# Optimization experiments

Hardware: AMD Instinct MI355X
Metric: run time of the kernel (lower is better)

Reference implementation:

```python
import jax, jax.numpy as jnp
import numpy as np

N_INST = 524288   # total instances across all bags
NF = 256          # feature dim
L = 128           # gated-attention hidden dim
C = 1             # num_classes
B = 4096          # num bags


def setup_inputs() -> dict:
    key = jax.random.key(0)
    k = jax.random.split(key, 6)
    # ragged bag sizes averaging ~128, deterministically summing to N_INST
    rng = np.random.RandomState(0)
    raw = rng.randint(64, 193, size=B).astype(np.int64)
    sizes = (raw * N_INST // raw.sum()).astype(np.int64)
    sizes[: int(N_INST - sizes.sum())] += 1  # distribute remainder (< B)
    assert sizes.sum() == N_INST
    s = 1.0 / np.sqrt(NF)
    return {
        "feats": jax.random.normal(k[0], (N_INST, NF), jnp.float32),
        "split_sizes": jnp.asarray(sizes, jnp.int64),
        "W_ins": jax.random.normal(k[1], (NF, C), jnp.float32) * s,
        "b_ins": jnp.zeros((C,), jnp.float32),
        "W_V": jax.random.normal(k[2], (NF, L), jnp.float32) * s,
        "b_V": jnp.zeros((L,), jnp.float32),
        "W_U": jax.random.normal(k[3], (NF, L), jnp.float32) * s,
        "b_U": jnp.zeros((L,), jnp.float32),
        "w_att": jax.random.normal(k[4], (L, 1), jnp.float32) * (1.0 / np.sqrt(L)),
        "b_att": jnp.zeros((1,), jnp.float32),
    }


def reference(feats, split_sizes, W_ins, b_ins, W_V, b_V, W_U, b_U, w_att, b_att):
    n = feats.shape[0]
    num_bags = split_sizes.shape[0]
    # segment id per instance (fused replacement of torch.split + Python loop)
    seg = jnp.repeat(jnp.arange(num_bags), split_sizes, total_repeat_length=n)

    # instance classifier (applied once to the whole ragged batch)
    inst_pred = feats @ W_ins + b_ins                      # [N, C]

    # gated attention scores
    gate = jnp.tanh(feats @ W_V + b_V) * jax.nn.sigmoid(feats @ W_U + b_U)
    scores = (gate @ w_att + b_att)[:, 0]                  # [N]

    # segmented softmax over each bag
    m = jax.ops.segment_max(scores, seg, num_segments=num_bags)  # [B]
    e = jnp.exp(scores - m[seg])
    denom = jax.ops.segment_sum(e, seg, num_segments=num_bags)   # [B]
    attn = e / denom[seg]                                        # [N]

    # bag prediction = attention-weighted sum of instance predictions
    bag_pred = jax.ops.segment_sum(attn[:, None] * inst_pred, seg,
                                   num_segments=num_bags)        # [B, C]
    return bag_pred, inst_pred
```

## Files before the change

kernel.cpp:

```cpp
#include <hip/hip_runtime.h>
#include <hip/hip_bf16.h>

#define N_INST 524288
#define NF     256
#define LDIM   128
#define NBAGS  4096

typedef __attribute__((ext_vector_type(8)))  short          short8;
typedef __attribute__((ext_vector_type(16))) float          f32x16;
typedef __attribute__((ext_vector_type(4)))  unsigned short ushort4v;
typedef __attribute__((ext_vector_type(4)))  int            int4v;

__device__ __forceinline__ unsigned short f2bf(float f) {
    unsigned u = __float_as_uint(f);
    unsigned r = u + 0x7FFFu + ((u >> 16) & 1u);
    return (unsigned short)(r >> 16);
}

__global__ __launch_bounds__(256) void k_build(const float* __restrict__ W_V,
                                               const float* __restrict__ W_U,
                                               unsigned short* __restrict__ Bws) {
    int idx  = blockIdx.x * 256 + threadIdx.x;
    int j    = idx & 7;
    int lane = (idx >> 3) & 63;
    int ct   = (idx >> 9) & 7;
    int ks   = idx >> 12;
    int k    = ks * 16 + ((lane >> 5) << 3) + j;
    int n    = ((ct >> 1) << 5) + (lane & 31);
    const float* src = (ct & 1) ? W_U : W_V;
    Bws[idx] = f2bf(src[k * LDIM + n]);
}

__global__ __launch_bounds__(256) void k_scan(const int* __restrict__ sraw,
                                              int* __restrict__ offs) {
    __shared__ int csum[256];
    __shared__ int cpref[256];
    const int t = threadIdx.x;
    const bool is64 = (sraw[1] == 0);
    int local[16];
    int ssum = 0;
    for (int j = 0; j < 16; ++j) {
        int i = t * 16 + j;
        int v = is64 ? sraw[2 * i] : sraw[i];
        local[j] = v;
        ssum += v;
    }
    csum[t] = ssum;
    __syncthreads();
    if (t == 0) {
        int run = 0;
        for (int i = 0; i < 256; ++i) { cpref[i] = run; run += csum[i]; }
    }
    __syncthreads();
    int run = cpref[t];
    for (int j = 0; j < 16; ++j) { offs[t * 16 + j] = run; run += local[j]; }
    if (t == 255) offs[NBAGS] = run;
}

__global__ __launch_bounds__(256, 3) void k_gemm(
    const float* __restrict__ feats, const unsigned short* __restrict__ Bws,
    const float* __restrict__ W_ins, const float* __restrict__ b_ins,
    const float* __restrict__ b_V,   const float* __restrict__ b_U,
    const float* __restrict__ w_att, const float* __restrict__ b_att,
    float* __restrict__ scores, float* __restrict__ inst_out) {

    __shared__ unsigned short Al[1024];
    __shared__ unsigned short Bl[4096];
    __shared__ float winsl[NF];
    __shared__ float bVl[LDIM], bUl[LDIM], wal[LDIM];
    __shared__ float Sp[64][4];

    const int t    = threadIdx.x;
    const int lane = t & 63;
    const int cg   = t >> 6;
    const int row  = t >> 2;
    const int seg  = t & 3;
    const long r0  = (long)blockIdx.x * 64;

    winsl[t] = W_ins[t];
    if (t < LDIM) { bVl[t] = b_V[t]; bUl[t] = b_U[t]; wal[t] = w_att[t]; }

    f32x16 acc[2][2] = {};
    float pacc = 0.f;

    const float* arow = feats + (r0 + row) * NF + seg * 4;
    const int4v* bsrc = (const int4v*)Bws;
    const int aoff = (((row >> 5) * 64) + ((seg >> 1) * 32) + (row & 31)) * 8
                     + (seg & 1) * 4;

    for (int ks = 0; ks < 16; ++ks) {
        __syncthreads();
        float4 av = *(const float4*)(arow + ks * 16);
        float4 wv = *(const float4*)&winsl[ks * 16 + seg * 4];
        pacc += av.x * wv.x + av.y * wv.y + av.z * wv.z + av.w * wv.w;
        ushort4v a4;
        a4.x = f2bf(av.x); a4.y = f2bf(av.y); a4.z = f2bf(av.z); a4.w = f2bf(av.w);
        *(ushort4v*)&Al[aoff] = a4;
        ((int4v*)Bl)[t]       = bsrc[ks * 512 + t];
        ((int4v*)Bl)[t + 256] = bsrc[ks * 512 + t + 256];
        __syncthreads();

        short8 a0 = *(const short8*)&Al[(0 * 64 + lane) * 8];
        short8 a1 = *(const short8*)&Al[(1 * 64 + lane) * 8];
        short8 bv = *(const short8*)&Bl[((cg * 2 + 0) * 64 + lane) * 8];
        short8 bu = *(const short8*)&Bl[((cg * 2 + 1) * 64 + lane) * 8];
        acc[0][0] = __builtin_amdgcn_mfma_f32_32x32x16_bf16(a0, bv, acc[0][0], 0, 0, 0);
        acc[0][1] = __builtin_amdgcn_mfma_f32_32x32x16_bf16(a0, bu, acc[0][1], 0, 0, 0);
        acc[1][0] = __builtin_amdgcn_mfma_f32_32x32x16_bf16(a1, bv, acc[1][0], 0, 0, 0);
        acc[1][1] = __builtin_amdgcn_mfma_f32_32x32x16_bf16(a1, bu, acc[1][1], 0, 0, 0);
    }

    const int   c32 = lane & 31;
    const int   n   = cg * 32 + c32;
    const float bv0 = bVl[n], bu0 = bUl[n], wn = wal[n];
    const int   rh  = lane >> 5;
    #pragma unroll
    for (int rt = 0; rt < 2; ++rt) {
        float s[16];
        #pragma unroll
        for (int r = 0; r < 16; ++r) {
            float v  = acc[rt][0][r] + bv0;
            float u  = acc[rt][1][r] + bu0;
            float ev = __expf(2.f * v);
            float th = 1.f - 2.f * __builtin_amdgcn_rcpf(ev + 1.f);
            float sg = __builtin_amdgcn_rcpf(1.f + __expf(-u));
            s[r] = th * sg * wn;
        }
        #pragma unroll
        for (int r = 0; r < 16; ++r) {
            float x = s[r];
            x += __shfl_xor(x, 1);
            x += __shfl_xor(x, 2);
            x += __shfl_xor(x, 4);
            x += __shfl_xor(x, 8);
            x += __shfl_xor(x, 16);
            s[r] = x;
        }
        if (c32 == 0) {
            #pragma unroll
            for (int r = 0; r < 16; ++r) {
                int rl = (r & 3) + 8 * (r >> 2) + 4 * rh;
                Sp[rt * 32 + rl][cg] = s[r];
            }
        }
    }

    float pt = pacc;
    pt += __shfl_xor(pt, 1);
    pt += __shfl_xor(pt, 2);
    if (seg == 0) inst_out[r0 + row] = pt + b_ins[0];

    __syncthreads();
    if (t < 64)
        scores[r0 + t] = Sp[t][0] + Sp[t][1] + Sp[t][2] + Sp[t][3] + b_att[0];
}

__global__ __launch_bounds__(64) void k_bags(const int* __restrict__ offs,
                                             const float* __restrict__ scores,
                                             const float* __restrict__ inst,
                                             float* __restrict__ bag_out) {
    const int b    = blockIdx.x;
    const int lane = threadIdx.x;
    const int s0 = offs[b], s1 = offs[b + 1];
    float m = -1e30f;
    for (int i = s0 + lane; i < s1; i += 64) m = fmaxf(m, scores[i]);
    #pragma unroll
    for (int d = 32; d; d >>= 1) m = fmaxf(m, __shfl_xor(m, d));
    float se = 0.f, sp = 0.f;
    for (int i = s0 + lane; i < s1; i += 64) {
        float e = __expf(scores[i] - m);
        se += e;
        sp += e * inst[i];
    }
    #pragma unroll
    for (int d = 32; d; d >>= 1) { se += __shfl_xor(se, d); sp += __shfl_xor(sp, d); }
    if (lane == 0) bag_out[b] = sp / se;
}

extern "C" void kernel_launch(void* const* d_in, const int* in_sizes, int n_in,
                              void* d_out, int out_size, void* d_ws, size_t ws_size,
                              hipStream_t stream) {
    const float* feats  = (const float*)d_in[0];
    const int*   sizesr = (const int*)d_in[1];
    const float* W_ins  = (const float*)d_in[2];
    const float* b_ins  = (const float*)d_in[3];
    const float* W_V    = (const float*)d_in[4];
    const float* b_V    = (const float*)d_in[5];
    const float* W_U    = (const float*)d_in[6];
    const float* b_U    = (const float*)d_in[7];
    const float* w_att  = (const float*)d_in[8];
    const float* b_att  = (const float*)d_in[9];

    unsigned short* Bws    = (unsigned short*)d_ws;
    int*            offs   = (int*)((char*)d_ws + (128 << 10));
    float*          scores = (float*)((char*)d_ws + (160 << 10));

    float* bag_out  = (float*)d_out;
    float* inst_out = (float*)d_out + NBAGS;

    hipLaunchKernelGGL(k_build, dim3(256), dim3(256), 0, stream, W_V, W_U, Bws);
    hipLaunchKernelGGL(k_scan,  dim3(1),   dim3(256), 0, stream, sizesr, offs);
    hipLaunchKernelGGL(k_gemm,  dim3(N_INST / 64), dim3(256), 0, stream,
                       feats, Bws, W_ins, b_ins, b_V, b_U, w_att, b_att,
                       scores, inst_out);
    hipLaunchKernelGGL(k_bags,  dim3(NBAGS), dim3(64), 0, stream,
                       offs, scores, inst_out, bag_out);
}
```

Before: 910.5 us.

## Double-buffer LDS with register prefetch and widen GEMM tile to 128 rows

The GEMM kernel now processes 128 instances per block instead of 64, so each B-tile load from global/LDS is reused across four MFMA row tiles. It double-buffers the A and B LDS tiles and prefetches the next two k-slices into registers, which removes one barrier per iteration and overlaps global loads with MFMA work. The cost is higher register pressure: launch bounds drop to 2 blocks per CU and there are eight accumulators. Grid size halves accordingly.

Result: faster. 887.3 us (-2.6%).

```diff
diff --git a/kernel.cpp b/kernel.cpp
--- a/kernel.cpp
+++ b/kernel.cpp
@@ -5,6 +5,7 @@
 #define NF     256
 #define LDIM   128
 #define NBAGS  4096
+#define BM     128
 
 typedef __attribute__((ext_vector_type(8)))  short          short8;
 typedef __attribute__((ext_vector_type(16))) float          f32x16;
@@ -57,101 +58,149 @@
     if (t == 255) offs[NBAGS] = run;
 }
 
-__global__ __launch_bounds__(256, 3) void k_gemm(
+__global__ __launch_bounds__(256, 2) void k_gemm(
     const float* __restrict__ feats, const unsigned short* __restrict__ Bws,
     const float* __restrict__ W_ins, const float* __restrict__ b_ins,
     const float* __restrict__ b_V,   const float* __restrict__ b_U,
     const float* __restrict__ w_att, const float* __restrict__ b_att,
     float* __restrict__ scores, float* __restrict__ inst_out) {
 
-    __shared__ unsigned short Al[1024];
-    __shared__ unsigned short Bl[4096];
+    __shared__ unsigned short Al[2][2048];
+    __shared__ unsigned short Bl[2][4096];
     __shared__ float winsl[NF];
     __shared__ float bVl[LDIM], bUl[LDIM], wal[LDIM];
-    __shared__ float Sp[64][4];
+    __shared__ float Sp[BM][4];
 
     const int t    = threadIdx.x;
     const int lane = t & 63;
     const int cg   = t >> 6;
-    const int row  = t >> 2;
-    const int seg  = t & 3;
-    const long r0  = (long)blockIdx.x * 64;
+    const long r0  = (long)blockIdx.x * BM;
+
+    const int row0 = t >> 2;
+    const int q    = t & 3;
+    const int row1 = row0 + 64;
 
     winsl[t] = W_ins[t];
     if (t < LDIM) { bVl[t] = b_V[t]; bUl[t] = b_U[t]; wal[t] = w_att[t]; }
 
-    f32x16 acc[2][2] = {};
-    float pacc = 0.f;
-
-    const float* arow = feats + (r0 + row) * NF + seg * 4;
-    const int4v* bsrc = (const int4v*)Bws;
-    const int aoff = (((row >> 5) * 64) + ((seg >> 1) * 32) + (row & 31)) * 8
-                     + (seg & 1) * 4;
-
+    const float* arow0 = feats + (r0 + row0) * NF + q * 4;
+    const float* arow1 = feats + (r0 + row1) * NF + q * 4;
+    const int4v* bsrc  = (const int4v*)Bws;
+
+    const int aoff0 = ((row0 >> 5) * 64 + (q >> 1) * 32 + (row0 & 31)) * 8 + (q & 1) * 4;
+    const int aoff1 = ((row1 >> 5) * 64 + (q >> 1) * 32 + (row1 & 31)) * 8 + (q & 1) * 4;
+
+    float4 pa0_0 = *(const float4*)(arow0);
+    float4 pa1_0 = *(const float4*)(arow1);
+    int4v  pb0_0 = bsrc[t];
+    int4v  pb1_0 = bsrc[t + 256];
+    float4 pa0_1 = *(const float4*)(arow0 + 16);
+    float4 pa1_1 = *(const float4*)(arow1 + 16);
+    int4v  pb0_1 = bsrc[512 + t];
+    int4v  pb1_1 = bsrc[512 + t + 256];
+
+    f32x16 accV0 = {}, accV1 = {}, accV2 = {}, accV3 = {};
+    f32x16 accU0 = {}, accU1 = {}, accU2 = {}, accU3 = {};
+    float pacc0 = 0.f, pacc1 = 0.f;
+
+    __syncthreads();
+
+    #pragma unroll
     for (int ks = 0; ks < 16; ++ks) {
-        __syncthreads();
-        float4 av = *(const float4*)(arow + ks * 16);
-        float4 wv = *(const float4*)&winsl[ks * 16 + seg * 4];
-        pacc += av.x * wv.x + av.y * wv.y + av.z * wv.z + av.w * wv.w;
-        ushort4v a4;
-        a4.x = f2bf(av.x); a4.y = f2bf(av.y); a4.z = f2bf(av.z); a4.w = f2bf(av.w);
-        *(ushort4v*)&Al[aoff] = a4;
-        ((int4v*)Bl)[t]       = bsrc[ks * 512 + t];
-        ((int4v*)Bl)[t + 256] = bsrc[ks * 512 + t + 256];
-        __syncthreads();
-
-        short8 a0 = *(const short8*)&Al[(0 * 64 + lane) * 8];
-        short8 a1 = *(const short8*)&Al[(1 * 64 + lane) * 8];
-        short8 bv = *(const short8*)&Bl[((cg * 2 + 0) * 64 + lane) * 8];
-        short8 bu = *(const short8*)&Bl[((cg * 2 + 1) * 64 + lane) * 8];
-        acc[0][0] = __builtin_amdgcn_mfma_f32_32x32x16_bf16(a0, bv, acc[0][0], 0, 0, 0);
-        acc[0][1] = __builtin_amdgcn_mfma_f32_32x32x16_bf16(a0, bu, acc[0][1], 0, 0, 0);
-        acc[1][0] = __builtin_amdgcn_mfma_f32_32x32x16_bf16(a1, bv, acc[1][0], 0, 0, 0);
-        acc[1][1] = __builtin_amdgcn_mfma_f32_32x32x16_bf16(a1, bu, acc[1][1], 0, 0, 0);
-    }
-
-    const int   c32 = lane & 31;
-    const int   n   = cg * 32 + c32;
-    const float bv0 = bVl[n], bu0 = bUl[n], wn = wal[n];
-    const int   rh  = lane >> 5;
-    #pragma unroll
-    for (int rt = 0; rt < 2; ++rt) {
-        float s[16];
-        #pragma unroll
-        for (int r = 0; r < 16; ++r) {
-            float v  = acc[rt][0][r] + bv0;
-            float u  = acc[rt][1][r] + bu0;
-            float ev = __expf(2.f * v);
-            float th = 1.f - 2.f * __builtin_amdgcn_rcpf(ev + 1.f);
-            float sg = __builtin_amdgcn_rcpf(1.f + __expf(-u));
-            s[r] = th * sg * wn;
-        }
-        #pragma unroll
-        for (int r = 0; r < 16; ++r) {
-            float x = s[r];
-            x += __shfl_xor(x, 1);
-            x += __shfl_xor(x, 2);
-            x += __shfl_xor(x, 4);
-            x += __shfl_xor(x, 8);
-            x += __shfl_xor(x, 16);
-            s[r] = x;
-        }
-        if (c32 == 0) {
-            #pragma unroll
-            for (int r = 0; r < 16; ++r) {
-                int rl = (r & 3) + 8 * (r >> 2) + 4 * rh;
-                Sp[rt * 32 + rl][cg] = s[r];
+        float4 av0 = (ks & 1) ? pa0_1 : pa0_0;
+        float4 av1 = (ks & 1) ? pa1_1 : pa1_0;
+        int4v  bv0 = (ks & 1) ? pb0_1 : pb0_0;
+        int4v  bv1 = (ks & 1) ? pb1_1 : pb1_0;
+        const int X = ks & 1;
+
+        float4 wv = *(const float4*)&winsl[ks * 16 + q * 4];
+        pacc0 += av0.x * wv.x + av0.y * wv.y + av0.z * wv.z + av0.w * wv.w;
+        pacc1 += av1.x * wv.x + av1.y * wv.y + av1.z * wv.z + av1.w * wv.w;
+
+        ushort4v c0, c1;
+        c0.x = f2bf(av0.x); c0.y = f2bf(av0.y); c0.z = f2bf(av0.z); c0.w = f2bf(av0.w);
+        c1.x = f2bf(av1.x); c1.y = f2bf(av1.y); c1.z = f2bf(av1.z); c1.w = f2bf(av1.w);
+        *(ushort4v*)&Al[X][aoff0] = c0;
+        *(ushort4v*)&Al[X][aoff1] = c1;
+        ((int4v*)Bl[X])[t]       = bv0;
+        ((int4v*)Bl[X])[t + 256] = bv1;
+
+        if (ks < 14) {
+            if (X == 0) {
+                pa0_0 = *(const float4*)(arow0 + (ks + 2) * 16);
+                pa1_0 = *(const float4*)(arow1 + (ks + 2) * 16);
+                pb0_0 = bsrc[(ks + 2) * 512 + t];
+                pb1_0 = bsrc[(ks + 2) * 512 + t + 256];
+            } else {
+                pa0_1 = *(const float4*)(arow0 + (ks + 2) * 16);
+                pa1_1 = *(const float4*)(arow1 + (ks + 2) * 16);
+                pb0_1 = bsrc[(ks + 2) * 512 + t];
+                pb1_1 = bsrc[(ks + 2) * 512 + t + 256];
             }
         }
-    }
-
-    float pt = pacc;
-    pt += __shfl_xor(pt, 1);
-    pt += __shfl_xor(pt, 2);
-    if (seg == 0) inst_out[r0 + row] = pt + b_ins[0];
-
-    __syncthreads();
-    if (t < 64)
+
+        __syncthreads();
+
+        short8 fa0 = *(const short8*)&Al[X][(0 * 64 + lane) * 8];
+        short8 fa1 = *(const short8*)&Al[X][(1 * 64 + lane) * 8];
+        short8 fa2 = *(const short8*)&Al[X][(2 * 64 + lane) * 8];
+        short8 fa3 = *(const short8*)&Al[X][(3 * 64 + lane) * 8];
+        short8 fbv = *(const short8*)&Bl[X][((cg * 2 + 0) * 64 + lane) * 8];
+        short8 fbu = *(const short8*)&Bl[X][((cg * 2 + 1) * 64 + lane) * 8];
+        accV0 = __builtin_amdgcn_mfma_f32_32x32x16_bf16(fa0, fbv, accV0, 0, 0, 0);
+        accU0 = __builtin_amdgcn_mfma_f32_32x32x16_bf16(fa0, fbu, accU0, 0, 0, 0);
+        accV1 = __builtin_amdgcn_mfma_f32_32x32x16_bf16(fa1, fbv, accV1, 0, 0, 0);
+        accU1 = __builtin_amdgcn_mfma_f32_32x32x16_bf16(fa1, fbu, accU1, 0, 0, 0);
+        accV2 = __builtin_amdgcn_mfma_f32_32x32x16_bf16(fa2, fbv, accV2, 0, 0, 0);
+        accU2 = __builtin_amdgcn_mfma_f32_32x32x16_bf16(fa2, fbu, accU2, 0, 0, 0);
+        accV3 = __builtin_amdgcn_mfma_f32_32x32x16_bf16(fa3, fbv, accV3, 0, 0, 0);
+        accU3 = __builtin_amdgcn_mfma_f32_32x32x16_bf16(fa3, fbu, accU3, 0, 0, 0);
+    }
+
+    const int   c32 = lane & 31;
+    const int   nn  = cg * 32 + c32;
+    const float bv0s = bVl[nn], bu0s = bUl[nn], wn = wal[nn];
+    const int   rh  = lane >> 5;
+
+#define EPILOG(RT, AV, AU)                                                    \
+    {                                                                         \
+        _Pragma("unroll")                                                     \
+        for (int r = 0; r < 16; ++r) {                                        \
+            float v  = AV[r] + bv0s;                                          \
+            float u  = AU[r] + bu0s;                                          \
+            float ev = __expf(2.f * v);                                       \
+            float th = 1.f - 2.f * __builtin_amdgcn_rcpf(ev + 1.f);           \
+            float sg = __builtin_amdgcn_rcpf(1.f + __expf(-u));               \
+            float x  = th * sg * wn;                                          \
+            x += __shfl_xor(x, 1);                                            \
+            x += __shfl_xor(x, 2);                                            \
+            x += __shfl_xor(x, 4);                                            \
+            x += __shfl_xor(x, 8);                                            \
+            x += __shfl_xor(x, 16);                                           \
+            if (c32 == 0)                                                     \
+                Sp[RT * 32 + (r & 3) + 8 * (r >> 2) + 4 * rh][cg] = x;        \
+        }                                                                     \
+    }
+    EPILOG(0, accV0, accU0)
+    EPILOG(1, accV1, accU1)
+    EPILOG(2, accV2, accU2)
+    EPILOG(3, accV3, accU3)
+#undef EPILOG
+
+    float pt0 = pacc0;
+    pt0 += __shfl_xor(pt0, 1);
+    pt0 += __shfl_xor(pt0, 2);
+    float pt1 = pacc1;
+    pt1 += __shfl_xor(pt1, 1);
+    pt1 += __shfl_xor(pt1, 2);
+    if (q == 0) {
+        float bi = b_ins[0];
+        inst_out[r0 + row0] = pt0 + bi;
+        inst_out[r0 + row1] = pt1 + bi;
+    }
+
+    __syncthreads();
+    if (t < BM)
         scores[r0 + t] = Sp[t][0] + Sp[t][1] + Sp[t][2] + Sp[t][3] + b_att[0];
 }
 
@@ -200,7 +249,7 @@
 
     hipLaunchKernelGGL(k_build, dim3(256), dim3(256), 0, stream, W_V, W_U, Bws);
     hipLaunchKernelGGL(k_scan,  dim3(1),   dim3(256), 0, stream, sizesr, offs);
-    hipLaunchKernelGGL(k_gemm,  dim3(N_INST / 64), dim3(256), 0, stream,
+    hipLaunchKernelGGL(k_gemm,  dim3(N_INST / BM), dim3(256), 0, stream,
                        feats, Bws, W_ins, b_ins, b_V, b_U, w_att, b_att,
                        scores, inst_out);
     hipLaunchKernelGGL(k_bags,  dim3(NBAGS), dim3(64), 0, stream,
```
